# Performance work log

Hardware: AMD Instinct MI355X
Metric: run time of the kernel (lower is better)

## Reference

```python
import jax, jax.numpy as jnp
import numpy as np

N = 100000   # nodes
E = 1600000  # edges
D = 128      # input_dim == hidden_dim
L = 3        # n_layers
P = 7        # n_properties
B = 64       # graphs in batch
BN_EPS = 1e-5
NEG_SLOPE = 0.2


def setup_inputs() -> dict:
    key = jax.random.key(0)
    ks = jax.random.split(key, 18)
    s = 1.0 / np.sqrt(D)
    sp = 1.0 / np.sqrt(P)
    return {
        "x": jax.random.normal(ks[0], (N, D), jnp.float32),
        "edge_index": jax.random.randint(ks[1], (2, E), 0, N, dtype=jnp.int64),
        "batch": jnp.sort(jax.random.randint(ks[2], (N,), 0, B, dtype=jnp.int64)),
        "graph_stats": jax.random.normal(ks[3], (B, P), jnp.float32),
        # GIN MLP params (stacked over layers; input_dim == hidden_dim == D)
        "W1s": jax.random.normal(ks[4], (L, D, D), jnp.float32) * s,
        "b1s": jnp.zeros((L, D), jnp.float32),
        "gammas": jnp.ones((L, D), jnp.float32),
        "betas": jnp.zeros((L, D), jnp.float32),
        "bn_means": jax.random.normal(ks[5], (L, D), jnp.float32) * 0.1,
        "bn_vars": jax.random.uniform(ks[6], (L, D), jnp.float32) + 0.5,
        "W2s": jax.random.normal(ks[7], (L, D, D), jnp.float32) * s,
        "b2s": jnp.zeros((L, D), jnp.float32),
        # stat conditioning transforms
        "statWs": jax.random.normal(ks[8], (L, P, D), jnp.float32) * sp,
        "statBs": jnp.zeros((L, D), jnp.float32),
        # fc_out
        "fcW": jax.random.normal(ks[9], (D, D), jnp.float32) * s,
        "fcB": jnp.zeros((D,), jnp.float32),
    }


def reference(x, edge_index, batch, graph_stats,
              W1s, b1s, gammas, betas, bn_means, bn_vars, W2s, b2s,
              statWs, statBs, fcW, fcB):
    # per-node graph stats (nan -> -100, then broadcast by graph id)
    node_stats = jnp.nan_to_num(graph_stats, nan=-100.0)[batch]  # [N, P]
    src, dst = edge_index[0], edge_index[1]
    h = x
    for i in range(L):
        # GIN aggregation (eps = 0): (1+eps)*h_i + sum_{j->i} h_j
        agg = jax.ops.segment_sum(h[src], dst, num_segments=N)  # [N, D]
        m = h + agg
        # MLP: Linear -> LeakyReLU(0.2) -> BatchNorm1d (eval) -> Linear -> LeakyReLU(0.2)
        m = jax.nn.leaky_relu(m @ W1s[i] + b1s[i], NEG_SLOPE)
        m = (m - bn_means[i]) * (gammas[i] / jnp.sqrt(bn_vars[i] + BN_EPS)) + betas[i]
        m = jax.nn.leaky_relu(m @ W2s[i] + b2s[i], NEG_SLOPE)
        # stats conditioning add (dropout is identity in eval mode)
        h = m + node_stats @ statWs[i] + statBs[i]
    return h @ fcW + fcB  # [N, D]
```

## Files before the change

### kernel.cpp

```cpp
#include <hip/hip_runtime.h>
#include <math.h>

#define N_NODES 100000
#define N_EDGES 1600000
#define D 128
#define L_LAYERS 3
#define P_STATS 7
#define B_GRAPHS 64
#define BN_EPS 1e-5f
#define NEG_SLOPE 0.2f

#define NB 196
#define BCAP 10240
#define EPB 6400

typedef __attribute__((ext_vector_type(8))) short bf16x8;
typedef __attribute__((ext_vector_type(4))) float f32x4;

static __device__ __forceinline__ short f2bf(float f) {
    union { float f; unsigned u; } v;
    v.f = f;
    unsigned r = v.u + 0x7fffu + ((v.u >> 16) & 1u);
    return (short)(r >> 16);
}

static __device__ __forceinline__ float bf2f(short s) {
    union { unsigned u; float f; } v;
    v.u = ((unsigned)(unsigned short)s) << 16;
    return v.f;
}


__global__ void zero_n_kernel(int* __restrict__ p, int n) {
    int i = blockIdx.x * blockDim.x + threadIdx.x;
    if (i < n) p[i] = 0;
}

__global__ __launch_bounds__(256) void bucketA_kernel(const int* __restrict__ src,
                                                      const int* __restrict__ dst,
                                                      int* __restrict__ bucket_cnt,
                                                      int2* __restrict__ bucketbuf) {
    __shared__ int s_src[EPB];
    __shared__ int s_dst[EPB];
    __shared__ int hist[NB], base[NB], loc[NB];
    const int tid = threadIdx.x;
    const int e0 = blockIdx.x * EPB;
    for (int i = tid; i < NB; i += 256) { hist[i] = 0; loc[i] = 0; }
    __syncthreads();
    for (int i = tid; i < EPB; i += 256) {
        int s = src[e0 + i];
        int d = dst[e0 + i];
        s_src[i] = s;
        s_dst[i] = d;
        atomicAdd(&hist[d >> 9], 1);
    }
    __syncthreads();
    for (int i = tid; i < NB; i += 256)
        base[i] = hist[i] ? atomicAdd(&bucket_cnt[i], hist[i]) : 0;
    __syncthreads();
    for (int i = tid; i < EPB; i += 256) {
        int d = s_dst[i];
        int b = d >> 9;
        int off = atomicAdd(&loc[b], 1);
        int idx = base[b] + off;
        if (idx < BCAP) bucketbuf[(size_t)b * BCAP + idx] = make_int2(s_src[i], d);
    }
}

__global__ __launch_bounds__(256) void bucketB1_kernel(const int* __restrict__ bucket_cnt,
                                                       const int2* __restrict__ bucketbuf,
                                                       int* __restrict__ deg) {
    __shared__ int hist[512];
    const int b = blockIdx.x;
    for (int i = threadIdx.x; i < 512; i += 256) hist[i] = 0;
    __syncthreads();
    int cnt = min(bucket_cnt[b], BCAP);
    for (int i = threadIdx.x; i < cnt; i += 256) {
        int d = bucketbuf[(size_t)b * BCAP + i].y;
        atomicAdd(&hist[d & 511], 1);
    }
    __syncthreads();
    int nbase = b << 9;
    for (int i = threadIdx.x; i < 512; i += 256) {
        int node = nbase + i;
        if (node < N_NODES) deg[node] = hist[i];
    }
}

__global__ __launch_bounds__(256) void bucketB2_kernel(const int* __restrict__ bucket_cnt,
                                                       const int2* __restrict__ bucketbuf,
                                                       int* __restrict__ cursor,
                                                       int* __restrict__ csr_src) {
    const int b = blockIdx.x;
    int cnt = min(bucket_cnt[b], BCAP);
    for (int i = threadIdx.x; i < cnt; i += 256) {
        int2 p = bucketbuf[(size_t)b * BCAP + i];
        int pos = atomicAdd(&cursor[p.y], 1);
        csr_src[pos] = p.x;
    }
}


__global__ void scan1_kernel(const int* __restrict__ deg, int* __restrict__ incl,
                             int* __restrict__ bsum) {
    __shared__ int s[256];
    const int tid = threadIdx.x;
    const int base = blockIdx.x * 2048;
    int v[8];
    int sum = 0;
    const int idx0 = base + tid * 8;
#pragma unroll
    for (int i = 0; i < 8; ++i) {
        int idx = idx0 + i;
        int d = (idx < N_NODES) ? deg[idx] : 0;
        sum += d;
        v[i] = sum;
    }
    s[tid] = sum;
    __syncthreads();
    for (int off = 1; off < 256; off <<= 1) {
        int t = (tid >= off) ? s[tid - off] : 0;
        __syncthreads();
        s[tid] += t;
        __syncthreads();
    }
    int prev = (tid > 0) ? s[tid - 1] : 0;
#pragma unroll
    for (int i = 0; i < 8; ++i) {
        int idx = idx0 + i;
        if (idx < N_NODES) incl[idx] = v[i] + prev;
    }
    if (tid == 255) bsum[blockIdx.x] = s[255];
}

__global__ void scan2_kernel(int* __restrict__ bsum, int nb) {
    if (threadIdx.x == 0 && blockIdx.x == 0) {
        int run = 0;
        for (int i = 0; i < nb; ++i) { int t = bsum[i]; bsum[i] = run; run += t; }
    }
}

__global__ void scan3_kernel(const int* __restrict__ deg, const int* __restrict__ incl,
                             const int* __restrict__ bsum, int* __restrict__ start,
                             int* __restrict__ cursor) {
    int i = blockIdx.x * blockDim.x + threadIdx.x;
    if (i < N_NODES) {
        int inc = incl[i] + bsum[i >> 11];
        int st = inc - deg[i];
        start[i] = st;
        cursor[i] = st;
    }
    if (i == 0) start[N_NODES] = N_EDGES;
}

__global__ void gproj_kernel(const float* __restrict__ gs, const float* __restrict__ statWs,
                             const float* __restrict__ statBs, float* __restrict__ gproj) {
    int b = blockIdx.x;
    int l = blockIdx.y;
    int j = threadIdx.x;
    float acc = statBs[l * D + j];
#pragma unroll
    for (int p = 0; p < P_STATS; ++p) {
        float g = gs[b * P_STATS + p];
        if (g != g) g = -100.0f;
        acc += g * statWs[(l * P_STATS + p) * D + j];
    }
    gproj[(l * B_GRAPHS + b) * D + j] = acc;
}

__global__ void wconv_kernel(const float* __restrict__ W1s, const float* __restrict__ W2s,
                             const float* __restrict__ fcW, short* __restrict__ wt) {
    int mid = blockIdx.y;
    const float* src = (mid < 3) ? (W1s + mid * D * D)
                                 : ((mid < 6) ? (W2s + (mid - 3) * D * D) : fcW);
    short* dstm = wt + mid * D * D;
    int i = blockIdx.x * 256 + threadIdx.x;
    int k = i >> 7, n = i & 127;
    dstm[n * D + k] = f2bf(src[i]);
}

__global__ __launch_bounds__(256) void xconv_kernel(const float* __restrict__ x,
                                                    short* __restrict__ xb) {
    int i = blockIdx.x * 256 + threadIdx.x;
    const float4* x4 = (const float4*)x;
    float4 a = x4[i * 2], b = x4[i * 2 + 1];
    short s[8];
    s[0] = f2bf(a.x); s[1] = f2bf(a.y); s[2] = f2bf(a.z); s[3] = f2bf(a.w);
    s[4] = f2bf(b.x); s[5] = f2bf(b.y); s[6] = f2bf(b.z); s[7] = f2bf(b.w);
    *(bf16x8*)&xb[i * 8] = *(bf16x8*)s;
}

template <bool FUSE_FC>
__global__ __launch_bounds__(256, 6) void mlp_fused_kernel(
    const short* __restrict__ h_in,
    const int* __restrict__ start, const int* __restrict__ csr_src,
    const short* __restrict__ W1t,
    const float* __restrict__ b1,
    const float* __restrict__ gamma, const float* __restrict__ beta,
    const float* __restrict__ mean, const float* __restrict__ var,
    const short* __restrict__ W2t,
    const float* __restrict__ b2,
    const float* __restrict__ gproj, const int* __restrict__ batch,
    const short* __restrict__ Wft, const float* __restrict__ fcb,
    float* __restrict__ outf, short* __restrict__ outb) {
    __shared__ short sy[64 * 128];
    __shared__ float sB1[128], sSc[128], sSb[128], sB2[128], sFC[128];

    const int tid = threadIdx.x;
    const int wid = tid >> 6;
    const int lane = tid & 63;
    const int lr = lane & 15;
    const int lk = lane >> 4;

    if (tid < 128) {
        sB1[tid] = b1[tid];
        float sc = gamma[tid] * rsqrtf(var[tid] + BN_EPS);
        sSc[tid] = sc;
        sSb[tid] = beta[tid] - mean[tid] * sc;
        sB2[tid] = b2[tid];
        if (FUSE_FC) sFC[tid] = fcb[tid];
    }

    {
        const bf16x8* h8 = (const bf16x8*)h_in;
        const int c8 = lane & 15;
        const int sub = lane >> 4;
#pragma unroll
        for (int it = 0; it < 4; ++it) {
            int nl = wid * 16 + it * 4 + sub;
            int node = blockIdx.x * 64 + nl;
            float acc[8];
            if (node < N_NODES) {
                bf16x8 own = h8[node * 16 + c8];
#pragma unroll
                for (int i = 0; i < 8; ++i) acc[i] = bf2f(own[i]);
                int s = start[node];
                int e = start[node + 1];
                int k = s;
                for (; k + 4 <= e; k += 4) {
                    int sn0 = csr_src[k];
                    int sn1 = csr_src[k + 1];
                    int sn2 = csr_src[k + 2];
                    int sn3 = csr_src[k + 3];
                    bf16x8 v0 = h8[sn0 * 16 + c8];
                    bf16x8 v1 = h8[sn1 * 16 + c8];
                    bf16x8 v2 = h8[sn2 * 16 + c8];
                    bf16x8 v3 = h8[sn3 * 16 + c8];
#pragma unroll
                    for (int i = 0; i < 8; ++i) acc[i] += bf2f(v0[i]);
#pragma unroll
                    for (int i = 0; i < 8; ++i) acc[i] += bf2f(v1[i]);
#pragma unroll
                    for (int i = 0; i < 8; ++i) acc[i] += bf2f(v2[i]);
#pragma unroll
                    for (int i = 0; i < 8; ++i) acc[i] += bf2f(v3[i]);
                }
                for (; k < e; ++k) {
                    int sn0 = csr_src[k];
                    bf16x8 v0 = h8[sn0 * 16 + c8];
#pragma unroll
                    for (int i = 0; i < 8; ++i) acc[i] += bf2f(v0[i]);
                }
            } else {
#pragma unroll
                for (int i = 0; i < 8; ++i) acc[i] = 0.f;
            }
            short pk[8];
#pragma unroll
            for (int i = 0; i < 8; ++i) pk[i] = f2bf(acc[i]);
            int byteoff = nl * 256 + c8 * 16;
            byteoff ^= (nl & 7) << 4;
            *(bf16x8*)((char*)sy + byteoff) = *(bf16x8*)pk;
        }
    }
    __syncthreads();

    const int nlBase = (wid >> 1) * 32;
    const int nodeBase = blockIdx.x * 64 + nlBase;
    const int featBase = (wid & 1) * 64;

    int nIdx[2];
#pragma unroll
    for (int mt = 0; mt < 2; ++mt) {
        int n = nodeBase + mt * 16 + lr;
        nIdx[mt] = (n < N_NODES) ? n : (N_NODES - 1);
    }

    f32x4 acc[4][2];
#pragma unroll
    for (int ft = 0; ft < 4; ++ft)
#pragma unroll
        for (int mt = 0; mt < 2; ++mt)
            acc[ft][mt] = (f32x4)(0.0f);

#pragma unroll
    for (int kt = 0; kt < 4; ++kt) {
        bf16x8 wfk[4];
#pragma unroll
        for (int ft = 0; ft < 4; ++ft)
            wfk[ft] = *(const bf16x8*)&W1t[(featBase + ft * 16 + lr) * D + kt * 32 + lk * 8];
        bf16x8 mf[2];
#pragma unroll
        for (int mt = 0; mt < 2; ++mt) {
            int nl = nlBase + mt * 16 + lr;
            int byteoff = nl * 256 + kt * 64 + lk * 16;
            byteoff ^= (nl & 7) << 4;
            mf[mt] = *(const bf16x8*)((char*)sy + byteoff);
        }
#pragma unroll
        for (int ft = 0; ft < 4; ++ft)
#pragma unroll
            for (int mt = 0; mt < 2; ++mt)
                acc[ft][mt] = __builtin_amdgcn_mfma_f32_16x16x32_bf16(wfk[ft], mf[mt],
                                                                      acc[ft][mt], 0, 0, 0);
    }
    __syncthreads();

#pragma unroll
    for (int ft = 0; ft < 4; ++ft) {
        int f0 = featBase + ft * 16 + lk * 4;
#pragma unroll
        for (int mt = 0; mt < 2; ++mt) {
            int nl = nlBase + mt * 16 + lr;
            short4 pk;
#pragma unroll
            for (int r = 0; r < 4; ++r) {
                float v = acc[ft][mt][r] + sB1[f0 + r];
                v = (v > 0.f) ? v : NEG_SLOPE * v;
                v = v * sSc[f0 + r] + sSb[f0 + r];
                ((short*)&pk)[r] = f2bf(v);
            }
            int byteoff = nl * 256 + f0 * 2;
            byteoff ^= (nl & 7) << 4;
            *(short4*)((char*)sy + byteoff) = pk;
        }
    }
    __syncthreads();

#pragma unroll
    for (int ft = 0; ft < 4; ++ft)
#pragma unroll
        for (int mt = 0; mt < 2; ++mt)
            acc[ft][mt] = (f32x4)(0.0f);

#pragma unroll
    for (int kt = 0; kt < 4; ++kt) {
        bf16x8 wfk[4];
#pragma unroll
        for (int ft = 0; ft < 4; ++ft)
            wfk[ft] = *(const bf16x8*)&W2t[(featBase + ft * 16 + lr) * D + kt * 32 + lk * 8];
        bf16x8 yf[2];
#pragma unroll
        for (int mt = 0; mt < 2; ++mt) {
            int nl = nlBase + mt * 16 + lr;
            int byteoff = nl * 256 + kt * 64 + lk * 16;
            byteoff ^= (nl & 7) << 4;
            yf[mt] = *(const bf16x8*)((char*)sy + byteoff);
        }
#pragma unroll
        for (int ft = 0; ft < 4; ++ft)
#pragma unroll
            for (int mt = 0; mt < 2; ++mt)
                acc[ft][mt] = __builtin_amdgcn_mfma_f32_16x16x32_bf16(wfk[ft], yf[mt],
                                                                      acc[ft][mt], 0, 0, 0);
    }

    if (!FUSE_FC) {
#pragma unroll
        for (int mt = 0; mt < 2; ++mt) {
            int node = nodeBase + mt * 16 + lr;
            if (node >= N_NODES) continue;
            int bid = batch[node];
#pragma unroll
            for (int ft = 0; ft < 4; ++ft) {
                int f0 = featBase + ft * 16 + lk * 4;
                const float4 gp = *(const float4*)&gproj[bid * D + f0];
                float v0 = acc[ft][mt][0] + sB2[f0 + 0]; v0 = (v0 > 0.f) ? v0 : NEG_SLOPE * v0; v0 += gp.x;
                float v1 = acc[ft][mt][1] + sB2[f0 + 1]; v1 = (v1 > 0.f) ? v1 : NEG_SLOPE * v1; v1 += gp.y;
                float v2 = acc[ft][mt][2] + sB2[f0 + 2]; v2 = (v2 > 0.f) ? v2 : NEG_SLOPE * v2; v2 += gp.z;
                float v3 = acc[ft][mt][3] + sB2[f0 + 3]; v3 = (v3 > 0.f) ? v3 : NEG_SLOPE * v3; v3 += gp.w;
                short4 pk;
                pk.x = f2bf(v0); pk.y = f2bf(v1); pk.z = f2bf(v2); pk.w = f2bf(v3);
                *(short4*)&outb[node * D + f0] = pk;
            }
        }
        return;
    }

    __syncthreads();
#pragma unroll
    for (int ft = 0; ft < 4; ++ft) {
        int f0 = featBase + ft * 16 + lk * 4;
#pragma unroll
        for (int mt = 0; mt < 2; ++mt) {
            int nl = nlBase + mt * 16 + lr;
            int bid = batch[nIdx[mt]];
            const float4 gp = *(const float4*)&gproj[bid * D + f0];
            short4 pk;
            float v0 = acc[ft][mt][0] + sB2[f0 + 0]; v0 = (v0 > 0.f) ? v0 : NEG_SLOPE * v0; v0 += gp.x;
            float v1 = acc[ft][mt][1] + sB2[f0 + 1]; v1 = (v1 > 0.f) ? v1 : NEG_SLOPE * v1; v1 += gp.y;
            float v2 = acc[ft][mt][2] + sB2[f0 + 2]; v2 = (v2 > 0.f) ? v2 : NEG_SLOPE * v2; v2 += gp.z;
            float v3 = acc[ft][mt][3] + sB2[f0 + 3]; v3 = (v3 > 0.f) ? v3 : NEG_SLOPE * v3; v3 += gp.w;
            pk.x = f2bf(v0); pk.y = f2bf(v1); pk.z = f2bf(v2); pk.w = f2bf(v3);
            int byteoff = nl * 256 + f0 * 2;
            byteoff ^= (nl & 7) << 4;
            *(short4*)((char*)sy + byteoff) = pk;
        }
    }
    __syncthreads();

#pragma unroll
    for (int ft = 0; ft < 4; ++ft)
#pragma unroll
        for (int mt = 0; mt < 2; ++mt)
            acc[ft][mt] = (f32x4)(0.0f);

#pragma unroll
    for (int kt = 0; kt < 4; ++kt) {
        bf16x8 wfk[4];
#pragma unroll
        for (int ft = 0; ft < 4; ++ft)
            wfk[ft] = *(const bf16x8*)&Wft[(featBase + ft * 16 + lr) * D + kt * 32 + lk * 8];
        bf16x8 hf[2];
#pragma unroll
        for (int mt = 0; mt < 2; ++mt) {
            int nl = nlBase + mt * 16 + lr;
            int byteoff = nl * 256 + kt * 64 + lk * 16;
            byteoff ^= (nl & 7) << 4;
            hf[mt] = *(const bf16x8*)((char*)sy + byteoff);
        }
#pragma unroll
        for (int ft = 0; ft < 4; ++ft)
#pragma unroll
            for (int mt = 0; mt < 2; ++mt)
                acc[ft][mt] = __builtin_amdgcn_mfma_f32_16x16x32_bf16(wfk[ft], hf[mt],
                                                                      acc[ft][mt], 0, 0, 0);
    }

#pragma unroll
    for (int mt = 0; mt < 2; ++mt) {
        int node = nodeBase + mt * 16 + lr;
        if (node >= N_NODES) continue;
#pragma unroll
        for (int ft = 0; ft < 4; ++ft) {
            int f0 = featBase + ft * 16 + lk * 4;
            float4 o;
            o.x = acc[ft][mt][0] + sFC[f0 + 0];
            o.y = acc[ft][mt][1] + sFC[f0 + 1];
            o.z = acc[ft][mt][2] + sFC[f0 + 2];
            o.w = acc[ft][mt][3] + sFC[f0 + 3];
            *(float4*)&outf[node * D + f0] = o;
        }
    }
}


extern "C" void kernel_launch(void* const* d_in, const int* in_sizes, int n_in,
                              void* d_out, int out_size, void* d_ws, size_t ws_size,
                              hipStream_t stream) {
    const float* x = (const float*)d_in[0];
    const int* ei = (const int*)d_in[1];
    const int* src = ei;
    const int* dst = ei + N_EDGES;
    const int* batch = (const int*)d_in[2];
    const float* gs = (const float*)d_in[3];
    const float* W1s = (const float*)d_in[4];
    const float* b1s = (const float*)d_in[5];
    const float* gammas = (const float*)d_in[6];
    const float* betas = (const float*)d_in[7];
    const float* means = (const float*)d_in[8];
    const float* vars = (const float*)d_in[9];
    const float* W2s = (const float*)d_in[10];
    const float* b2s = (const float*)d_in[11];
    const float* statWs = (const float*)d_in[12];
    const float* statBs = (const float*)d_in[13];
    const float* fcW = (const float*)d_in[14];
    const float* fcB = (const float*)d_in[15];
    float* out = (float*)d_out;

    char* ws = (char*)d_ws;
    auto alloc = [&](size_t bytes) {
        char* p = ws;
        ws += (bytes + 255) / 256 * 256;
        return p;
    };
    int* deg = (int*)alloc(N_NODES * sizeof(int));
    int* incl = (int*)alloc(N_NODES * sizeof(int));
    int* bsum = (int*)alloc(64 * sizeof(int));
    int* start = (int*)alloc((N_NODES + 1) * sizeof(int));
    int* cursor = (int*)alloc(N_NODES * sizeof(int));
    int* csr_src = (int*)alloc(N_EDGES * sizeof(int));
    int* bucket_cnt = (int*)alloc(NB * sizeof(int));
    int2* bucketbuf = (int2*)alloc((size_t)NB * BCAP * sizeof(int2));
    float* gproj = (float*)alloc((size_t)L_LAYERS * B_GRAPHS * D * sizeof(float));
    short* wt = (short*)alloc((size_t)7 * D * D * sizeof(short));
    short* xb = (short*)alloc((size_t)N_NODES * D * sizeof(short));
    short* hb1 = (short*)alloc((size_t)N_NODES * D * sizeof(short));
    short* hb2 = (short*)alloc((size_t)N_NODES * D * sizeof(short));

    const int nscan = (N_NODES + 2047) / 2048;

    zero_n_kernel<<<1, 256, 0, stream>>>(bucket_cnt, NB);
    bucketA_kernel<<<N_EDGES / EPB, 256, 0, stream>>>(src, dst, bucket_cnt, bucketbuf);
    bucketB1_kernel<<<NB, 256, 0, stream>>>(bucket_cnt, bucketbuf, deg);
    scan1_kernel<<<nscan, 256, 0, stream>>>(deg, incl, bsum);
    scan2_kernel<<<1, 64, 0, stream>>>(bsum, nscan);
    scan3_kernel<<<(N_NODES + 255) / 256, 256, 0, stream>>>(deg, incl, bsum, start, cursor);
    bucketB2_kernel<<<NB, 256, 0, stream>>>(bucket_cnt, bucketbuf, cursor, csr_src);

    gproj_kernel<<<dim3(B_GRAPHS, L_LAYERS), D, 0, stream>>>(gs, statWs, statBs, gproj);
    wconv_kernel<<<dim3(64, 7), 256, 0, stream>>>(W1s, W2s, fcW, wt);
    xconv_kernel<<<(N_NODES * D / 8 + 255) / 256, 256, 0, stream>>>(x, xb);

    const int mlp_blocks = (N_NODES + 63) / 64;

    mlp_fused_kernel<false><<<mlp_blocks, 256, 0, stream>>>(
        xb, start, csr_src, wt + 0 * D * D, b1s + 0 * D, gammas + 0 * D, betas + 0 * D,
        means + 0 * D, vars + 0 * D, wt + 3 * D * D, b2s + 0 * D, gproj + 0 * B_GRAPHS * D,
        batch, nullptr, nullptr, nullptr, hb1);
    mlp_fused_kernel<false><<<mlp_blocks, 256, 0, stream>>>(
        hb1, start, csr_src, wt + 1 * D * D, b1s + 1 * D, gammas + 1 * D, betas + 1 * D,
        means + 1 * D, vars + 1 * D, wt + 4 * D * D, b2s + 1 * D, gproj + 1 * B_GRAPHS * D,
        batch, nullptr, nullptr, nullptr, hb2);
    mlp_fused_kernel<true><<<mlp_blocks, 256, 0, stream>>>(
        hb2, start, csr_src, wt + 2 * D * D, b1s + 2 * D, gammas + 2 * D, betas + 2 * D,
        means + 2 * D, vars + 2 * D, wt + 5 * D * D, b2s + 2 * D, gproj + 2 * B_GRAPHS * D,
        batch, wt + 6 * D * D, fcB, out, nullptr);
}
```

Before: 436.8 us.

## Split aggregation into feature-sliced gather kernel with sliced activation layout

Stores node features in 8 feature slices of 16 bf16 each, so each slice is a compact 3.2 MB array. A separate aggregation kernel gathers one slice per block, so the random neighbour gathers hit a smaller working set that may stay in cache. The MLP kernel now reads aggregated rows from global memory instead of LDS. This adds an extra global round trip for the aggregated features plus an extra kernel launch per layer, and it reads the CSR index arrays eight times.

Measured after the change: 601.5 us. +37.7%, slower.

```diff
diff --git a/kernel.cpp b/kernel.cpp
--- a/kernel.cpp
+++ b/kernel.cpp
@@ -14,8 +14,12 @@
 #define BCAP 10240
 #define EPB 6400
 
+#define NSLICE 8
+#define SLICE_STRIDE ((size_t)N_NODES * 16)
+
 typedef __attribute__((ext_vector_type(8))) short bf16x8;
 typedef __attribute__((ext_vector_type(4))) float f32x4;
+typedef __attribute__((ext_vector_type(4))) int i32x4;
 
 static __device__ __forceinline__ short f2bf(float f) {
     union { float f; unsigned u; } v;
@@ -180,20 +184,77 @@
 }
 
 __global__ __launch_bounds__(256) void xconv_kernel(const float* __restrict__ x,
-                                                    short* __restrict__ xb) {
+                                                    short* __restrict__ xs) {
     int i = blockIdx.x * 256 + threadIdx.x;
-    const float4* x4 = (const float4*)x;
-    float4 a = x4[i * 2], b = x4[i * 2 + 1];
+    int node = i >> 4;
+    int part = i & 15;
+    const float4* x4 = (const float4*)&x[node * D + part * 8];
+    float4 a = x4[0], b = x4[1];
     short s[8];
     s[0] = f2bf(a.x); s[1] = f2bf(a.y); s[2] = f2bf(a.z); s[3] = f2bf(a.w);
     s[4] = f2bf(b.x); s[5] = f2bf(b.y); s[6] = f2bf(b.z); s[7] = f2bf(b.w);
-    *(bf16x8*)&xb[i * 8] = *(bf16x8*)s;
+    int slice = part >> 1;
+    int j = (part & 1) * 8;
+    *(bf16x8*)&xs[slice * SLICE_STRIDE + node * 16 + j] = *(bf16x8*)s;
+}
+
+__global__ __launch_bounds__(256) void agg_sliced_kernel(const short* __restrict__ h_s,
+                                                         const int* __restrict__ start,
+                                                         const int* __restrict__ csr_src,
+                                                         short* __restrict__ m_s) {
+    const int s = blockIdx.x & 7;
+    const int chunk = blockIdx.x >> 3;
+    const int lane = threadIdx.x & 63;
+    const int wave = threadIdx.x >> 6;
+    const int node = chunk * 128 + wave * 32 + (lane >> 1);
+    const int hb = lane & 1;
+    if (node >= N_NODES) return;
+
+    const bf16x8* h8 = (const bf16x8*)(h_s + (size_t)s * SLICE_STRIDE);
+    bf16x8 own = h8[node * 2 + hb];
+    float acc[8];
+#pragma unroll
+    for (int i = 0; i < 8; ++i) acc[i] = bf2f(own[i]);
+
+    int st = __builtin_nontemporal_load(&start[node]);
+    int en = __builtin_nontemporal_load(&start[node + 1]);
+    int k = st;
+    for (; k + 4 <= en; k += 4) {
+        int sn0 = __builtin_nontemporal_load(&csr_src[k]);
+        int sn1 = __builtin_nontemporal_load(&csr_src[k + 1]);
+        int sn2 = __builtin_nontemporal_load(&csr_src[k + 2]);
+        int sn3 = __builtin_nontemporal_load(&csr_src[k + 3]);
+        bf16x8 v0 = h8[sn0 * 2 + hb];
+        bf16x8 v1 = h8[sn1 * 2 + hb];
+        bf16x8 v2 = h8[sn2 * 2 + hb];
+        bf16x8 v3 = h8[sn3 * 2 + hb];
+#pragma unroll
+        for (int i = 0; i < 8; ++i) acc[i] += bf2f(v0[i]);
+#pragma unroll
+        for (int i = 0; i < 8; ++i) acc[i] += bf2f(v1[i]);
+#pragma unroll
+        for (int i = 0; i < 8; ++i) acc[i] += bf2f(v2[i]);
+#pragma unroll
+        for (int i = 0; i < 8; ++i) acc[i] += bf2f(v3[i]);
+    }
+    for (; k < en; ++k) {
+        int sn0 = __builtin_nontemporal_load(&csr_src[k]);
+        bf16x8 v0 = h8[sn0 * 2 + hb];
+#pragma unroll
+        for (int i = 0; i < 8; ++i) acc[i] += bf2f(v0[i]);
+    }
+
+    short pk[8];
+#pragma unroll
+    for (int i = 0; i < 8; ++i) pk[i] = f2bf(acc[i]);
+    i32x4 w = *(i32x4*)pk;
+    __builtin_nontemporal_store(w,
+        (i32x4*)(m_s + (size_t)s * SLICE_STRIDE + node * 16 + hb * 8));
 }
 
 template <bool FUSE_FC>
-__global__ __launch_bounds__(256, 6) void mlp_fused_kernel(
-    const short* __restrict__ h_in,
-    const int* __restrict__ start, const int* __restrict__ csr_src,
+__global__ __launch_bounds__(256, 4) void mlp_mfma_kernel(
+    const short* __restrict__ m_s,
     const short* __restrict__ W1t,
     const float* __restrict__ b1,
     const float* __restrict__ gamma, const float* __restrict__ beta,
@@ -202,7 +263,7 @@
     const float* __restrict__ b2,
     const float* __restrict__ gproj, const int* __restrict__ batch,
     const short* __restrict__ Wft, const float* __restrict__ fcb,
-    float* __restrict__ outf, short* __restrict__ outb) {
+    float* __restrict__ outf, short* __restrict__ outs) {
     __shared__ short sy[64 * 128];
     __shared__ float sB1[128], sSc[128], sSb[128], sB2[128], sFC[128];
 
@@ -220,59 +281,6 @@
         sB2[tid] = b2[tid];
         if (FUSE_FC) sFC[tid] = fcb[tid];
     }
-
-    {
-        const bf16x8* h8 = (const bf16x8*)h_in;
-        const int c8 = lane & 15;
-        const int sub = lane >> 4;
-#pragma unroll
-        for (int it = 0; it < 4; ++it) {
-            int nl = wid * 16 + it * 4 + sub;
-            int node = blockIdx.x * 64 + nl;
-            float acc[8];
-            if (node < N_NODES) {
-                bf16x8 own = h8[node * 16 + c8];
-#pragma unroll
-                for (int i = 0; i < 8; ++i) acc[i] = bf2f(own[i]);
-                int s = start[node];
-                int e = start[node + 1];
-                int k = s;
-                for (; k + 4 <= e; k += 4) {
-                    int sn0 = csr_src[k];
-                    int sn1 = csr_src[k + 1];
-                    int sn2 = csr_src[k + 2];
-                    int sn3 = csr_src[k + 3];
-                    bf16x8 v0 = h8[sn0 * 16 + c8];
-                    bf16x8 v1 = h8[sn1 * 16 + c8];
-                    bf16x8 v2 = h8[sn2 * 16 + c8];
-                    bf16x8 v3 = h8[sn3 * 16 + c8];
-#pragma unroll
-                    for (int i = 0; i < 8; ++i) acc[i] += bf2f(v0[i]);
-#pragma unroll
-                    for (int i = 0; i < 8; ++i) acc[i] += bf2f(v1[i]);
-#pragma unroll
-                    for (int i = 0; i < 8; ++i) acc[i] += bf2f(v2[i]);
-#pragma unroll
-                    for (int i = 0; i < 8; ++i) acc[i] += bf2f(v3[i]);
-                }
-                for (; k < e; ++k) {
-                    int sn0 = csr_src[k];
-                    bf16x8 v0 = h8[sn0 * 16 + c8];
-#pragma unroll
-                    for (int i = 0; i < 8; ++i) acc[i] += bf2f(v0[i]);
-                }
-            } else {
-#pragma unroll
-                for (int i = 0; i < 8; ++i) acc[i] = 0.f;
-            }
-            short pk[8];
-#pragma unroll
-            for (int i = 0; i < 8; ++i) pk[i] = f2bf(acc[i]);
-            int byteoff = nl * 256 + c8 * 16;
-            byteoff ^= (nl & 7) << 4;
-            *(bf16x8*)((char*)sy + byteoff) = *(bf16x8*)pk;
-        }
-    }
     __syncthreads();
 
     const int nlBase = (wid >> 1) * 32;
@@ -299,14 +307,12 @@
 #pragma unroll
         for (int ft = 0; ft < 4; ++ft)
             wfk[ft] = *(const bf16x8*)&W1t[(featBase + ft * 16 + lr) * D + kt * 32 + lk * 8];
+        const int f = kt * 32 + lk * 8;
+        const short* mp = m_s + (size_t)(f >> 4) * SLICE_STRIDE + (f & 15);
         bf16x8 mf[2];
 #pragma unroll
-        for (int mt = 0; mt < 2; ++mt) {
-            int nl = nlBase + mt * 16 + lr;
-            int byteoff = nl * 256 + kt * 64 + lk * 16;
-            byteoff ^= (nl & 7) << 4;
-            mf[mt] = *(const bf16x8*)((char*)sy + byteoff);
-        }
+        for (int mt = 0; mt < 2; ++mt)
+            mf[mt] = *(const bf16x8*)(mp + nIdx[mt] * 16);
 #pragma unroll
         for (int ft = 0; ft < 4; ++ft)
 #pragma unroll
@@ -314,7 +320,6 @@
                 acc[ft][mt] = __builtin_amdgcn_mfma_f32_16x16x32_bf16(wfk[ft], mf[mt],
                                                                       acc[ft][mt], 0, 0, 0);
     }
-    __syncthreads();
 
 #pragma unroll
     for (int ft = 0; ft < 4; ++ft) {
@@ -381,7 +386,7 @@
                 float v3 = acc[ft][mt][3] + sB2[f0 + 3]; v3 = (v3 > 0.f) ? v3 : NEG_SLOPE * v3; v3 += gp.w;
                 short4 pk;
                 pk.x = f2bf(v0); pk.y = f2bf(v1); pk.z = f2bf(v2); pk.w = f2bf(v3);
-                *(short4*)&outb[node * D + f0] = pk;
+                *(short4*)&outs[(size_t)(f0 >> 4) * SLICE_STRIDE + node * 16 + (f0 & 15)] = pk;
             }
         }
         return;
@@ -494,9 +499,9 @@
     int2* bucketbuf = (int2*)alloc((size_t)NB * BCAP * sizeof(int2));
     float* gproj = (float*)alloc((size_t)L_LAYERS * B_GRAPHS * D * sizeof(float));
     short* wt = (short*)alloc((size_t)7 * D * D * sizeof(short));
-    short* xb = (short*)alloc((size_t)N_NODES * D * sizeof(short));
-    short* hb1 = (short*)alloc((size_t)N_NODES * D * sizeof(short));
-    short* hb2 = (short*)alloc((size_t)N_NODES * D * sizeof(short));
+    short* xs = (short*)alloc((size_t)N_NODES * D * sizeof(short));
+    short* ms = (short*)alloc((size_t)N_NODES * D * sizeof(short));
+    short* hs1 = (short*)alloc((size_t)N_NODES * D * sizeof(short));
 
     const int nscan = (N_NODES + 2047) / 2048;
 
@@ -510,20 +515,24 @@
 
     gproj_kernel<<<dim3(B_GRAPHS, L_LAYERS), D, 0, stream>>>(gs, statWs, statBs, gproj);
     wconv_kernel<<<dim3(64, 7), 256, 0, stream>>>(W1s, W2s, fcW, wt);
-    xconv_kernel<<<(N_NODES * D / 8 + 255) / 256, 256, 0, stream>>>(x, xb);
-
+    xconv_kernel<<<N_NODES * 16 / 256, 256, 0, stream>>>(x, xs);
+
+    const int agg_blocks = ((N_NODES + 127) / 128) * NSLICE;
     const int mlp_blocks = (N_NODES + 63) / 64;
 
-    mlp_fused_kernel<false><<<mlp_blocks, 256, 0, stream>>>(
-        xb, start, csr_src, wt + 0 * D * D, b1s + 0 * D, gammas + 0 * D, betas + 0 * D,
-        means + 0 * D, vars + 0 * D, wt + 3 * D * D, b2s + 0 * D, gproj + 0 * B_GRAPHS * D,
-        batch, nullptr, nullptr, nullptr, hb1);
-    mlp_fused_kernel<false><<<mlp_blocks, 256, 0, stream>>>(
-        hb1, start, csr_src, wt + 1 * D * D, b1s + 1 * D, gammas + 1 * D, betas + 1 * D,
-        means + 1 * D, vars + 1 * D, wt + 4 * D * D, b2s + 1 * D, gproj + 1 * B_GRAPHS * D,
-        batch, nullptr, nullptr, nullptr, hb2);
-    mlp_fused_kernel<true><<<mlp_blocks, 256, 0, stream>>>(
-        hb2, start, csr_src, wt + 2 * D * D, b1s + 2 * D, gammas + 2 * D, betas + 2 * D,
-        means + 2 * D, vars + 2 * D, wt + 5 * D * D, b2s + 2 * D, gproj + 2 * B_GRAPHS * D,
-        batch, wt + 6 * D * D, fcB, out, nullptr);
-}
+    agg_sliced_kernel<<<agg_blocks, 256, 0, stream>>>(xs, start, csr_src, ms);
+    mlp_mfma_kernel<false><<<mlp_blocks, 256, 0, stream>>>(
+        ms, wt + 0 * D * D, b1s + 0 * D, gammas + 0 * D, betas + 0 * D, means + 0 * D,
+        vars + 0 * D, wt + 3 * D * D, b2s + 0 * D, gproj + 0 * B_GRAPHS * D, batch,
+        nullptr, nullptr, nullptr, hs1);
+    agg_sliced_kernel<<<agg_blocks, 256, 0, stream>>>(hs1, start, csr_src, ms);
+    mlp_mfma_kernel<false><<<mlp_blocks, 256, 0, stream>>>(
+        ms, wt + 1 * D * D, b1s + 1 * D, gammas + 1 * D, betas + 1 * D, means + 1 * D,
+        vars + 1 * D, wt + 4 * D * D, b2s + 1 * D, gproj + 1 * B_GRAPHS * D, batch,
+        nullptr, nullptr, nullptr, xs);
+    agg_sliced_kernel<<<agg_blocks, 256, 0, stream>>>(xs, start, csr_src, ms);
+    mlp_mfma_kernel<true><<<mlp_blocks, 256, 0, stream>>>(
+        ms, wt + 2 * D * D, b1s + 2 * D, gammas + 2 * D, betas + 2 * D, means + 2 * D,
+        vars + 2 * D, wt + 5 * D * D, b2s + 2 * D, gproj + 2 * B_GRAPHS * D, batch,
+        wt + 6 * D * D, fcB, out, nullptr);
+}
```
